# Performance work log

Hardware: AMD Instinct MI355X
Metric: run time of the kernel (lower is better)

The kernel has to match this reference:

```python
import jax, jax.numpy as jnp
import numpy as np

NUM_EXPERTS = 64
TOP_K = 2
CAP_FACTOR = 1.0


def setup_inputs() -> dict:
    key = jax.random.key(0)
    k1, k2 = jax.random.split(key)
    x = jax.random.normal(k1, (8192, 4096), dtype=jnp.float32)
    wg = jax.random.normal(k2, (NUM_EXPERTS, 4096), dtype=jnp.float32) * 0.02
    return {"x": x, "wg": wg}


def reference(x, wg):
    # x: [S, M] tokens, wg: [E, M] gate weight (Linear, no bias)
    S, M = x.shape
    E, K = NUM_EXPERTS, TOP_K
    capacity = K * int(CAP_FACTOR * ((S + E - 1) // E))  # static

    logits = jnp.einsum('sm,em->se', x, wg)            # [S, E]
    gates = jax.nn.softmax(logits, axis=1)             # [S, E]
    _, topk_idx = jax.lax.top_k(logits, K)             # [S, K]

    masks = jax.nn.one_hot(topk_idx, E, dtype=x.dtype)  # [S, K, E]
    gates_s = jnp.einsum('se,ske->sk', gates, masks)    # [S, K]

    # load-balancing loss (fp32 path of load_balance)
    me = jnp.sum(gates, axis=0)                         # [E]
    ce = jnp.sum(masks[:, 0], axis=0)                   # [E]
    l_loss = jnp.sum(me * ce) * (E / (S * S))

    # capacity locations: cumsum-sub-one per k, offset by counts of earlier k's
    locs = jnp.cumsum(masks, axis=0) - 1.0              # [S, K, E]
    counts = jnp.sum(masks, axis=0)                     # [K, E]
    acc = jnp.concatenate([jnp.zeros((1, E), x.dtype),
                           jnp.cumsum(counts, axis=0)[:-1]], axis=0)  # [K, E]
    locs = locs + acc[None, :, :]
    loc_s = jnp.einsum('ske,ske->sk', locs, masks).astype(jnp.int32)  # [S, K]

    # postnorm gate normalization (top_k > 1)
    eps = jnp.finfo(gates_s.dtype).eps
    gates_n = gates_s / jnp.clip(jnp.sum(gates_s, axis=1, keepdims=True), eps)

    idx = topk_idx.astype(jnp.int32)                    # [S, K]
    valid = (loc_s >= 0) & (loc_s < capacity)           # [S, K]
    pos = jnp.where(valid, idx * capacity + loc_s, 0)   # [S, K] flat slot ids

    # encode: scatter tokens (unweighted, is_postnorm=True) into [E*capacity, M]
    contrib = jnp.where(valid[..., None], x[:, None, :], 0.0)  # [S, K, M]
    dispatched = jnp.zeros((E * capacity, M), x.dtype)
    dispatched = dispatched.at[pos.reshape(-1)].add(contrib.reshape(-1, M))

    # expert_fn = identity (world_size=1, routing pipeline is the op under test)
    expert_output = dispatched                          # [E*capacity, M]

    # decode: gather back and combine with normalized gates
    gathered = expert_output[pos.reshape(-1)].reshape(S, K, M)
    out = jnp.einsum('sk,skm->sm', gates_n * valid.astype(x.dtype), gathered)
    return out, l_loss
```

## Files before the change

### kernel.cpp

```cpp
#include <hip/hip_runtime.h>
#include <math.h>

#define S_TOK 8192
#define M_DIM 4096
#define NEXP 64
#define CAPACITY 256
#define NCHUNK 128
#define KS 16
#define KSL 256
#define BT 256
#define BK 32
#define NC (KSL / BK)

__global__ __launch_bounds__(256) void k_logits(
    const float* __restrict__ x, const float* __restrict__ wg,
    float* __restrict__ part)
{
    __shared__ float xs[2][BK * BT];
    __shared__ float wsl[2][BK * 64];
    const int tid = threadIdx.x;
    const int tile = blockIdx.x >> 4;
    const int ks   = blockIdx.x & 15;
    const int t0 = tile * BT;
    const int kb = ks * KSL;

    const int tx = tid & 7;
    const int ty = tid >> 3;

    float4 rx[8], rw[2];
    auto ld = [&](int kc) {
        #pragma unroll
        for (int i = 0; i < 8; ++i) {
            const int item = tid + 256 * i;
            const int r = item >> 3, kq = item & 7;
            rx[i] = *(const float4*)(x + (size_t)(t0 + r) * M_DIM + kc + 4 * kq);
        }
        #pragma unroll
        for (int i = 0; i < 2; ++i) {
            const int item = tid + 256 * i;
            const int r = item >> 3, kq = item & 7;
            rw[i] = *(const float4*)(wg + (size_t)r * M_DIM + kc + 4 * kq);
        }
    };
    auto st = [&](int buf) {
        #pragma unroll
        for (int i = 0; i < 8; ++i) {
            const int item = tid + 256 * i;
            const int r = item >> 3, kq = item & 7;
            const int quad = r >> 2, lo = r & 3;
            const float v[4] = {rx[i].x, rx[i].y, rx[i].z, rx[i].w};
            #pragma unroll
            for (int j = 0; j < 4; ++j)
                xs[buf][(4 * kq + j) * BT + ((quad ^ kq) << 2) + lo] = v[j];
        }
        #pragma unroll
        for (int i = 0; i < 2; ++i) {
            const int item = tid + 256 * i;
            const int r = item >> 3, kq = item & 7;
            const int quad = r >> 2, lo = r & 3;
            const float v[4] = {rw[i].x, rw[i].y, rw[i].z, rw[i].w};
            #pragma unroll
            for (int j = 0; j < 4; ++j)
                wsl[buf][(4 * kq + j) * 64 + ((quad ^ kq) << 2) + lo] = v[j];
        }
    };

    float acc[8][8] = {};
    ld(kb);
    st(0);
    __syncthreads();
    for (int c = 0; c < NC; ++c) {
        const int buf = c & 1;
        if (c + 1 < NC) ld(kb + (c + 1) * BK);
        #pragma unroll 4
        for (int kk = 0; kk < BK; ++kk) {
            const int sw = kk >> 2;
            const float4 a0 = *(const float4*)&xs [buf][kk * BT + (((2 * ty)     ^ sw) << 2)];
            const float4 a1 = *(const float4*)&xs [buf][kk * BT + (((2 * ty + 1) ^ sw) << 2)];
            const float4 b0 = *(const float4*)&wsl[buf][kk * 64 + (((2 * tx)     ^ sw) << 2)];
            const float4 b1 = *(const float4*)&wsl[buf][kk * 64 + (((2 * tx + 1) ^ sw) << 2)];
            const float av[8] = {a0.x, a0.y, a0.z, a0.w, a1.x, a1.y, a1.z, a1.w};
            const float bv[8] = {b0.x, b0.y, b0.z, b0.w, b1.x, b1.y, b1.z, b1.w};
            #pragma unroll
            for (int i = 0; i < 8; ++i)
                #pragma unroll
                for (int j = 0; j < 8; ++j)
                    acc[i][j] = fmaf(av[i], bv[j], acc[i][j]);
        }
        __syncthreads();
        if (c + 1 < NC) st(buf ^ 1);
        __syncthreads();
    }

    #pragma unroll
    for (int i = 0; i < 8; ++i) {
        float4 v0, v1;
        v0.x = acc[i][0]; v0.y = acc[i][1]; v0.z = acc[i][2]; v0.w = acc[i][3];
        v1.x = acc[i][4]; v1.y = acc[i][5]; v1.z = acc[i][6]; v1.w = acc[i][7];
        float* dst = part + ((size_t)ks * S_TOK + t0 + 8 * ty + i) * NEXP + 8 * tx;
        *(float4*)dst = v0;
        *(float4*)(dst + 4) = v1;
    }
}

__global__ __launch_bounds__(512) void k_gate(
    const float* __restrict__ part, float* __restrict__ me_g,
    int* __restrict__ idx0_g, int* __restrict__ idx1_g,
    float* __restrict__ gn0_g, float* __restrict__ gn1_g,
    int* __restrict__ rank0_g, int* __restrict__ rank1_g,
    int* __restrict__ cnt_g )
{
    __shared__ float me_sh[NEXP];
    __shared__ int e0_sh[64], e1_sh[64];
    const int tid = threadIdx.x;
    if (tid < NEXP) me_sh[tid] = 0.f;
    __syncthreads();

    const int wv = tid >> 6, lane = tid & 63;
    const int chunk = blockIdx.x;
    float me_acc = 0.f;
    for (int i = 0; i < 8; ++i) {
        const int tt = wv * 8 + i;
        const int t = chunk * 64 + tt;
        float lg = 0.f;
        #pragma unroll
        for (int s = 0; s < KS; ++s)
            lg += part[((size_t)s * S_TOK + t) * NEXP + lane];

        float v = lg; int id = lane;
        #pragma unroll
        for (int off = 32; off > 0; off >>= 1) {
            float v2 = __shfl_xor(v, off);
            int   i2 = __shfl_xor(id, off);
            if (v2 > v || (v2 == v && i2 < id)) { v = v2; id = i2; }
        }
        const float mx = v; const int i0 = id;

        const float p = expf(lg - mx);
        float sum = p;
        #pragma unroll
        for (int off = 32; off > 0; off >>= 1) sum += __shfl_xor(sum, off);
        me_acc += p / sum;

        float v1 = (lane == i0) ? -INFINITY : lg; int id1 = lane;
        #pragma unroll
        for (int off = 32; off > 0; off >>= 1) {
            float v2 = __shfl_xor(v1, off);
            int   i2 = __shfl_xor(id1, off);
            if (v2 > v1 || (v2 == v1 && i2 < id1)) { v1 = v2; id1 = i2; }
        }

        const float g0 = 1.0f / sum;
        const float g1 = expf(v1 - mx) / sum;
        const float den = fmaxf(g0 + g1, 1.1920929e-07f);
        if (lane == 0) {
            idx0_g[t] = i0;
            idx1_g[t] = id1;
            gn0_g[t] = g0 / den;
            gn1_g[t] = g1 / den;
            e0_sh[tt] = i0;
            e1_sh[tt] = id1;
        }
    }
    atomicAdd(&me_sh[lane], me_acc);
    __syncthreads();
    if (tid < NEXP) atomicAdd(&me_g[tid], me_sh[tid]);

    if (wv == 0) {
        const int s = chunk * 64 + lane;
        const int e0 = e0_sh[lane], e1 = e1_sh[lane];
        const unsigned long long lt = (1ull << lane) - 1ull;
        int r0 = 0, r1 = 0, c0 = 0, c1 = 0;
        #pragma unroll
        for (int e = 0; e < 64; ++e) {
            unsigned long long m0 = __ballot(e0 == e);
            unsigned long long m1 = __ballot(e1 == e);
            if (e0 == e) r0 = __popcll(m0 & lt);
            if (e1 == e) r1 = __popcll(m1 & lt);
            if (lane == e) { c0 = __popcll(m0); c1 = __popcll(m1); }
        }
        rank0_g[s] = r0;
        rank1_g[s] = r1;
        cnt_g[chunk * 64 + lane] = c0;
        cnt_g[NCHUNK * 64 + chunk * 64 + lane] = c1;
    }
}

__global__ __launch_bounds__(256) void k_scan(
    const int* __restrict__ cnt_g, int* __restrict__ base_g,
    int* __restrict__ tot0_g, const float* __restrict__ me_g,
    float* __restrict__ loss_out)
{
    const int wv = threadIdx.x >> 6, lane = threadIdx.x & 63;
    const int g = blockIdx.x * 4 + wv;
    const int k = g >> 6, e = g & 63;

    const int c0 = cnt_g[(k * NCHUNK + 2 * lane)     * 64 + e];
    const int c1 = cnt_g[(k * NCHUNK + 2 * lane + 1) * 64 + e];
    const int s = c0 + c1;
    int incl = s;
    #pragma unroll
    for (int d = 1; d < 64; d <<= 1) {
        int v = __shfl_up(incl, d);
        if (lane >= d) incl += v;
    }
    const int excl = incl - s;
    base_g[(k * NCHUNK + 2 * lane)     * 64 + e] = excl;
    base_g[(k * NCHUNK + 2 * lane + 1) * 64 + e] = excl + c0;
    const int total = __shfl(incl, 63);
    if (k == 0 && lane == 0) {
        tot0_g[e] = total;
        atomicAdd(loss_out, me_g[e] * (float)total * 9.5367431640625e-07f);
    }
}

__global__ __launch_bounds__(256) void k_out(
    const float* __restrict__ x,
    const int* __restrict__ idx0_g, const int* __restrict__ idx1_g,
    const float* __restrict__ gn0_g, const float* __restrict__ gn1_g,
    const int* __restrict__ rank0_g, const int* __restrict__ rank1_g,
    const int* __restrict__ base_g, const int* __restrict__ tot0_g,
    float* __restrict__ out)
{
    const int s = blockIdx.x;
    const int chunk = s >> 6;
    const int e0 = idx0_g[s], e1 = idx1_g[s];
    const int loc0 = base_g[chunk * 64 + e0] + rank0_g[s];
    const int loc1 = base_g[(NCHUNK + chunk) * 64 + e1] + rank1_g[s] + tot0_g[e1];
    float w = 0.f;
    if (loc0 < CAPACITY) w += gn0_g[s];
    if (loc1 < CAPACITY) w += gn1_g[s];

    const float4* xr = (const float4*)(x + (size_t)s * M_DIM);
    float4* o = (float4*)(out + (size_t)s * M_DIM);
    #pragma unroll
    for (int i = 0; i < 4; ++i) {
        float4 v = xr[threadIdx.x + 256 * i];
        v.x *= w; v.y *= w; v.z *= w; v.w *= w;
        o[threadIdx.x + 256 * i] = v;
    }
}

extern "C" void kernel_launch(void* const* d_in, const int* in_sizes, int n_in,
                              void* d_out, int out_size, void* d_ws, size_t ws_size,
                              hipStream_t stream)
{
    const float* x  = (const float*)d_in[0];
    const float* wg = (const float*)d_in[1];
    float* out = (float*)d_out;
    float* loss = out + (size_t)S_TOK * M_DIM;

    float* part = (float*)d_ws;
    float* me   = part + (size_t)KS * S_TOK * NEXP;
    int*  idx0  = (int*)(me + NEXP);
    int*  idx1  = idx0 + S_TOK;
    float* gn0  = (float*)(idx1 + S_TOK);
    float* gn1  = gn0 + S_TOK;
    int*  rank0 = (int*)(gn1 + S_TOK);
    int*  rank1 = rank0 + S_TOK;
    int*  cnt   = rank1 + S_TOK;
    int*  base  = cnt + 2 * NCHUNK * 64;
    int*  tot0  = base + 2 * NCHUNK * 64;

    hipMemsetAsync(me, 0, NEXP * sizeof(float), stream);
    hipMemsetAsync(loss, 0, sizeof(float), stream);

    k_logits<<<32 * KS, 256, 0, stream>>>(x, wg, part);
    k_gate<<<NCHUNK, 512, 0, stream>>>(part, me, idx0, idx1, gn0, gn1,
                                       rank0, rank1, cnt);
    k_scan<<<32, 256, 0, stream>>>(cnt, base, tot0, me, loss);
    k_out<<<S_TOK, 256, 0, stream>>>(x, idx0, idx1, gn0, gn1,
                                     rank0, rank1, base, tot0, out);
}
```

Before: 308.5 us.

## Stage logits GEMM tiles via direct global-to-LDS loads with pre-transposed gate weights

Adds a small kernel that transposes the gate weight to [K, E], then rewrites the logits GEMM staging to use global_load_lds so tiles go straight from global memory into shared memory, skipping the register round-trip and the scalar transposed LDS stores. The x tile is now stored token-major with an XOR swizzle, and the inner loop is restructured to read 4-wide k slices per token. This removes one barrier per iteration and the register pressure from the prefetch buffers, and adds an occupancy hint of 2 blocks. The cost is an extra kernel launch, a workspace buffer, and reliance on the async LDS load path and its synchronisation being correct.

```diff
diff --git a/kernel.cpp b/kernel.cpp
--- a/kernel.cpp
+++ b/kernel.cpp
@@ -1,5 +1,6 @@
 #include <hip/hip_runtime.h>
 #include <math.h>
+#include <stdint.h>
 
 #define S_TOK 8192
 #define M_DIM 4096
@@ -12,83 +13,90 @@
 #define BK 32
 #define NC (KSL / BK)
 
-__global__ __launch_bounds__(256) void k_logits(
-    const float* __restrict__ x, const float* __restrict__ wg,
+__global__ __launch_bounds__(256) void k_wt(
+    const float* __restrict__ wg, float* __restrict__ wgT)
+{
+    const int k = blockIdx.x * 4 + (threadIdx.x >> 6);
+    const int e = threadIdx.x & 63;
+    wgT[(size_t)k * NEXP + e] = wg[(size_t)e * M_DIM + k];
+}
+
+__global__ __launch_bounds__(256, 2) void k_logits(
+    const float* __restrict__ x, const float* __restrict__ wgT,
     float* __restrict__ part)
 {
     __shared__ float xs[2][BK * BT];
-    __shared__ float wsl[2][BK * 64];
+    __shared__ float ws[2][BK * NEXP];
     const int tid = threadIdx.x;
     const int tile = blockIdx.x >> 4;
     const int ks   = blockIdx.x & 15;
     const int t0 = tile * BT;
     const int kb = ks * KSL;
 
+    const int wv = tid >> 6, lane = tid & 63;
     const int tx = tid & 7;
     const int ty = tid >> 3;
 
-    float4 rx[8], rw[2];
-    auto ld = [&](int kc) {
-        #pragma unroll
-        for (int i = 0; i < 8; ++i) {
-            const int item = tid + 256 * i;
-            const int r = item >> 3, kq = item & 7;
-            rx[i] = *(const float4*)(x + (size_t)(t0 + r) * M_DIM + kc + 4 * kq);
-        }
-        #pragma unroll
-        for (int i = 0; i < 2; ++i) {
-            const int item = tid + 256 * i;
-            const int r = item >> 3, kq = item & 7;
-            rw[i] = *(const float4*)(wg + (size_t)r * M_DIM + kc + 4 * kq);
+    auto stage = [&](int buf, int kc) {
+        #pragma unroll
+        for (int q = 0; q < 8; ++q) {
+            const int r = wv * 8 + q;
+            const int tok = r * 8 + (lane >> 3);
+            const int bsrc = (lane & 7) ^ (r & 7);
+            __builtin_amdgcn_global_load_lds(
+                (const __attribute__((address_space(1))) void*)
+                    (x + (size_t)(t0 + tok) * M_DIM + kc + 4 * bsrc),
+                (__attribute__((address_space(3))) void*)(&xs[buf][r * 256]),
+                16, 0, 0);
+        }
+        #pragma unroll
+        for (int q = 0; q < 2; ++q) {
+            const int rw = wv * 2 + q;
+            __builtin_amdgcn_global_load_lds(
+                (const __attribute__((address_space(1))) void*)
+                    (wgT + (size_t)kc * NEXP + rw * 256 + lane * 4),
+                (__attribute__((address_space(3))) void*)(&ws[buf][rw * 256]),
+                16, 0, 0);
         }
     };
-    auto st = [&](int buf) {
-        #pragma unroll
-        for (int i = 0; i < 8; ++i) {
-            const int item = tid + 256 * i;
-            const int r = item >> 3, kq = item & 7;
-            const int quad = r >> 2, lo = r & 3;
-            const float v[4] = {rx[i].x, rx[i].y, rx[i].z, rx[i].w};
-            #pragma unroll
-            for (int j = 0; j < 4; ++j)
-                xs[buf][(4 * kq + j) * BT + ((quad ^ kq) << 2) + lo] = v[j];
-        }
-        #pragma unroll
-        for (int i = 0; i < 2; ++i) {
-            const int item = tid + 256 * i;
-            const int r = item >> 3, kq = item & 7;
-            const int quad = r >> 2, lo = r & 3;
-            const float v[4] = {rw[i].x, rw[i].y, rw[i].z, rw[i].w};
-            #pragma unroll
-            for (int j = 0; j < 4; ++j)
-                wsl[buf][(4 * kq + j) * 64 + ((quad ^ kq) << 2) + lo] = v[j];
-        }
-    };
 
     float acc[8][8] = {};
-    ld(kb);
-    st(0);
+    stage(0, kb);
     __syncthreads();
+
     for (int c = 0; c < NC; ++c) {
         const int buf = c & 1;
-        if (c + 1 < NC) ld(kb + (c + 1) * BK);
-        #pragma unroll 4
-        for (int kk = 0; kk < BK; ++kk) {
-            const int sw = kk >> 2;
-            const float4 a0 = *(const float4*)&xs [buf][kk * BT + (((2 * ty)     ^ sw) << 2)];
-            const float4 a1 = *(const float4*)&xs [buf][kk * BT + (((2 * ty + 1) ^ sw) << 2)];
-            const float4 b0 = *(const float4*)&wsl[buf][kk * 64 + (((2 * tx)     ^ sw) << 2)];
-            const float4 b1 = *(const float4*)&wsl[buf][kk * 64 + (((2 * tx + 1) ^ sw) << 2)];
-            const float av[8] = {a0.x, a0.y, a0.z, a0.w, a1.x, a1.y, a1.z, a1.w};
-            const float bv[8] = {b0.x, b0.y, b0.z, b0.w, b1.x, b1.y, b1.z, b1.w};
+        if (c + 1 < NC) stage(buf ^ 1, kb + (c + 1) * BK);
+
+        const float* xb = xs[buf];
+        const float* wb = ws[buf];
+        #pragma unroll
+        for (int kq = 0; kq < BK / 4; ++kq) {
+            float4 al[8];
             #pragma unroll
-            for (int i = 0; i < 8; ++i)
+            for (int i = 0; i < 8; ++i) {
+                const int tok = 8 * ty + i;
+                al[i] = *(const float4*)&xb[tok * 32 + ((kq ^ (ty & 7)) << 2)];
+            }
+            float4 bl[4], bh[4];
+            #pragma unroll
+            for (int kk = 0; kk < 4; ++kk) {
+                bl[kk] = *(const float4*)&wb[(4 * kq + kk) * NEXP + 8 * tx];
+                bh[kk] = *(const float4*)&wb[(4 * kq + kk) * NEXP + 8 * tx + 4];
+            }
+            #pragma unroll
+            for (int kk = 0; kk < 4; ++kk) {
+                const float bj[8] = {bl[kk].x, bl[kk].y, bl[kk].z, bl[kk].w,
+                                     bh[kk].x, bh[kk].y, bh[kk].z, bh[kk].w};
                 #pragma unroll
-                for (int j = 0; j < 8; ++j)
-                    acc[i][j] = fmaf(av[i], bv[j], acc[i][j]);
-        }
-        __syncthreads();
-        if (c + 1 < NC) st(buf ^ 1);
+                for (int i = 0; i < 8; ++i) {
+                    const float ai = ((const float*)&al[i])[kk];
+                    #pragma unroll
+                    for (int j = 0; j < 8; ++j)
+                        acc[i][j] = fmaf(ai, bj[j], acc[i][j]);
+                }
+            }
+        }
         __syncthreads();
     }
 
@@ -261,11 +269,13 @@
     int*  cnt   = rank1 + S_TOK;
     int*  base  = cnt + 2 * NCHUNK * 64;
     int*  tot0  = base + 2 * NCHUNK * 64;
+    float* wgT  = (float*)(tot0 + NEXP);
 
     hipMemsetAsync(me, 0, NEXP * sizeof(float), stream);
     hipMemsetAsync(loss, 0, sizeof(float), stream);
 
-    k_logits<<<32 * KS, 256, 0, stream>>>(x, wg, part);
+    k_wt<<<M_DIM / 4, 256, 0, stream>>>(wg, wgT);
+    k_logits<<<32 * KS, 256, 0, stream>>>(x, wgT, part);
     k_gate<<<NCHUNK, 512, 0, stream>>>(part, me, idx0, idx1, gn0, gn1,
                                        rank0, rank1, cnt);
     k_scan<<<32, 256, 0, stream>>>(cnt, base, tot0, me, loss);
```

Measured after the change: 357.2 us. 1.16x slower.

## Replace LDS-staged logits GEMM with direct register-level global loads

Applied to the files above, without the earlier changes.

Removes the shared-memory tiling and barriers from the gating logits kernel; each thread now loads its own x and wg row fragments directly from global memory into double-buffered registers and accumulates an 8x8 tile. This aims to cut LDS store/load and synchronization overhead. It trades that for redundant, poorly coalesced global reads (x rows re-read by 8 threads, wg by many) and higher register pressure.

```diff
diff --git a/kernel.cpp b/kernel.cpp
--- a/kernel.cpp
+++ b/kernel.cpp
@@ -1,5 +1,6 @@
 #include <hip/hip_runtime.h>
 #include <math.h>
+#include <stdint.h>
 
 #define S_TOK 8192
 #define M_DIM 4096
@@ -9,15 +10,12 @@
 #define KS 16
 #define KSL 256
 #define BT 256
-#define BK 32
-#define NC (KSL / BK)
+#define NG (KSL / 4)
 
 __global__ __launch_bounds__(256) void k_logits(
     const float* __restrict__ x, const float* __restrict__ wg,
     float* __restrict__ part)
 {
-    __shared__ float xs[2][BK * BT];
-    __shared__ float wsl[2][BK * 64];
     const int tid = threadIdx.x;
     const int tile = blockIdx.x >> 4;
     const int ks   = blockIdx.x & 15;
@@ -27,70 +25,48 @@
     const int tx = tid & 7;
     const int ty = tid >> 3;
 
-    float4 rx[8], rw[2];
-    auto ld = [&](int kc) {
-        #pragma unroll
-        for (int i = 0; i < 8; ++i) {
-            const int item = tid + 256 * i;
-            const int r = item >> 3, kq = item & 7;
-            rx[i] = *(const float4*)(x + (size_t)(t0 + r) * M_DIM + kc + 4 * kq);
-        }
-        #pragma unroll
-        for (int i = 0; i < 2; ++i) {
-            const int item = tid + 256 * i;
-            const int r = item >> 3, kq = item & 7;
-            rw[i] = *(const float4*)(wg + (size_t)r * M_DIM + kc + 4 * kq);
-        }
+    const float* xrow[8];
+    const float* wrow[8];
+    #pragma unroll
+    for (int i = 0; i < 8; ++i)
+        xrow[i] = x + (size_t)(t0 + 8 * ty + i) * M_DIM + kb;
+    #pragma unroll
+    for (int j = 0; j < 8; ++j)
+        wrow[j] = wg + (size_t)(8 * tx + j) * M_DIM + kb;
+
+    float acc[8][8] = {};
+    float4 A0[8], B0[8], A1[8], B1[8];
+
+    auto loadg = [&](int g, float4* A, float4* B) {
+        #pragma unroll
+        for (int i = 0; i < 8; ++i)
+            A[i] = *(const float4*)(xrow[i] + 4 * g);
+        #pragma unroll
+        for (int j = 0; j < 8; ++j)
+            B[j] = *(const float4*)(wrow[j] + 4 * g);
     };
-    auto st = [&](int buf) {
-        #pragma unroll
-        for (int i = 0; i < 8; ++i) {
-            const int item = tid + 256 * i;
-            const int r = item >> 3, kq = item & 7;
-            const int quad = r >> 2, lo = r & 3;
-            const float v[4] = {rx[i].x, rx[i].y, rx[i].z, rx[i].w};
+    auto fmag = [&](const float4* A, const float4* B) {
+        #pragma unroll
+        for (int i = 0; i < 8; ++i)
             #pragma unroll
-            for (int j = 0; j < 4; ++j)
-                xs[buf][(4 * kq + j) * BT + ((quad ^ kq) << 2) + lo] = v[j];
-        }
-        #pragma unroll
-        for (int i = 0; i < 2; ++i) {
-            const int item = tid + 256 * i;
-            const int r = item >> 3, kq = item & 7;
-            const int quad = r >> 2, lo = r & 3;
-            const float v[4] = {rw[i].x, rw[i].y, rw[i].z, rw[i].w};
-            #pragma unroll
-            for (int j = 0; j < 4; ++j)
-                wsl[buf][(4 * kq + j) * 64 + ((quad ^ kq) << 2) + lo] = v[j];
-        }
+            for (int j = 0; j < 8; ++j) {
+                acc[i][j] = fmaf(A[i].x, B[j].x, acc[i][j]);
+                acc[i][j] = fmaf(A[i].y, B[j].y, acc[i][j]);
+                acc[i][j] = fmaf(A[i].z, B[j].z, acc[i][j]);
+                acc[i][j] = fmaf(A[i].w, B[j].w, acc[i][j]);
+            }
     };
 
-    float acc[8][8] = {};
-    ld(kb);
-    st(0);
-    __syncthreads();
-    for (int c = 0; c < NC; ++c) {
-        const int buf = c & 1;
-        if (c + 1 < NC) ld(kb + (c + 1) * BK);
-        #pragma unroll 4
-        for (int kk = 0; kk < BK; ++kk) {
-            const int sw = kk >> 2;
-            const float4 a0 = *(const float4*)&xs [buf][kk * BT + (((2 * ty)     ^ sw) << 2)];
-            const float4 a1 = *(const float4*)&xs [buf][kk * BT + (((2 * ty + 1) ^ sw) << 2)];
-            const float4 b0 = *(const float4*)&wsl[buf][kk * 64 + (((2 * tx)     ^ sw) << 2)];
-            const float4 b1 = *(const float4*)&wsl[buf][kk * 64 + (((2 * tx + 1) ^ sw) << 2)];
-            const float av[8] = {a0.x, a0.y, a0.z, a0.w, a1.x, a1.y, a1.z, a1.w};
-            const float bv[8] = {b0.x, b0.y, b0.z, b0.w, b1.x, b1.y, b1.z, b1.w};
-            #pragma unroll
-            for (int i = 0; i < 8; ++i)
-                #pragma unroll
-                for (int j = 0; j < 8; ++j)
-                    acc[i][j] = fmaf(av[i], bv[j], acc[i][j]);
-        }
-        __syncthreads();
-        if (c + 1 < NC) st(buf ^ 1);
-        __syncthreads();
-    }
+    loadg(0, A0, B0);
+    for (int g = 0; g < NG - 2; g += 2) {
+        loadg(g + 1, A1, B1);
+        fmag(A0, B0);
+        loadg(g + 2, A0, B0);
+        fmag(A1, B1);
+    }
+    loadg(NG - 1, A1, B1);
+    fmag(A0, B0);
+    fmag(A1, B1);
 
     #pragma unroll
     for (int i = 0; i < 8; ++i) {
```

New measurement: 396.9 us. +28.6%, slower.
